# Optimization experiments

Measured on AMD Instinct MI355X. Metric: run time of the kernel, lower is better.

## Reference

```python
import jax, jax.numpy as jnp
import numpy as np

B, K, L, D, H = 128, 51, 60, 1, 32
NB = 2  # MAF blocks
LOG2PI = float(np.log(2.0 * np.pi))


def setup_inputs():
    kit = iter(jax.random.split(jax.random.key(0), 64))
    def nrm(shape, s=0.05):
        return jax.random.normal(next(kit), shape, dtype=jnp.float32) * s
    def uni(shape, lo, hi):
        return jax.random.uniform(next(kit), shape, dtype=jnp.float32, minval=lo, maxval=hi)
    c = L * D          # attention feature dim = 60
    KL = K * L         # 3060
    KL32 = KL * 32     # 97920
    return dict(
        x=jax.random.normal(next(kit), (B, K, L, D), dtype=jnp.float32),
        attn_Wq=nrm((c, c), 0.1), attn_bq=nrm((c,), 0.1),
        attn_Wk=nrm((c, c), 0.1), attn_bk=nrm((c,), 0.1),
        lstm_Wih=nrm((4 * H, D), 0.2), lstm_Whh=nrm((4 * H, H), 0.1),
        lstm_bih=nrm((4 * H,), 0.1), lstm_bhh=nrm((4 * H,), 0.1),
        gnn_Wn=nrm((H, H), 0.1), gnn_bn=nrm((H,), 0.1),
        gnn_Wr=nrm((H, H), 0.1),
        gnn_W2=nrm((H, H), 0.1), gnn_b2=nrm((H,), 0.1),
        mlp_W1=nrm((KL, 500), 0.02), mlp_b1=nrm((500,), 0.05),
        bn1_g=uni((500,), 0.8, 1.2), bn1_b=nrm((500,), 0.05),
        bn1_m=nrm((500,), 0.05), bn1_v=uni((500,), 0.5, 1.5),
        mlp_W2=nrm((500, 500), 0.05), mlp_b2=nrm((500,), 0.05),
        bn2_g=uni((500,), 0.8, 1.2), bn2_b=nrm((500,), 0.05),
        bn2_m=nrm((500,), 0.05), bn2_v=uni((500,), 0.5, 1.5),
        mlp_W3=nrm((500, KL32), 0.05), mlp_b3=nrm((KL32,), 0.05),
        ann_W=nrm((KL32, 100), 0.005), ann_b=nrm((100,), 0.05),
        annbn_g=uni((100,), 0.8, 1.2), annbn_b=nrm((100,), 0.05),
        annbn_m=nrm((100,), 0.05), annbn_v=uni((100,), 0.5, 1.5),
        maf_in_W=nrm((NB, H, D), 0.1), maf_in_b=nrm((NB, H), 0.1),
        maf_cond_W=nrm((NB, H, H), 0.1),
        maf_out_W=nrm((NB, 2 * D, H), 0.1), maf_out_b=nrm((NB, 2 * D), 0.1),
        maf_bn_lg=nrm((NB, D), 0.05), maf_bn_beta=nrm((NB, D), 0.05),
    )


def _forward(x, attn_Wq, attn_bq, attn_Wk, attn_bk,
             lstm_Wih, lstm_Whh, lstm_bih, lstm_bhh,
             gnn_Wn, gnn_bn, gnn_Wr, gnn_W2, gnn_b2,
             mlp_W1, mlp_b1, bn1_g, bn1_b, bn1_m, bn1_v,
             mlp_W2, mlp_b2, bn2_g, bn2_b, bn2_m, bn2_v,
             mlp_W3, mlp_b3,
             ann_W, ann_b, annbn_g, annbn_b, annbn_m, annbn_v,
             maf_in_W, maf_in_b, maf_cond_W, maf_out_W, maf_out_b,
             maf_bn_lg, maf_bn_beta):
    Bb, Kk, Ll, Dd = x.shape
    c = Ll * Dd
    # --- ScaleDotProductAttention (eval: dropout = identity) ---
    xf = x.reshape(Bb, Kk, c)
    q = xf @ attn_Wq + attn_bq
    k = xf @ attn_Wk + attn_bk
    k_t = k.reshape(Bb, c, Kk)                 # torch .view -- a reshape, NOT a transpose
    score = (q @ k_t) / jnp.sqrt(jnp.asarray(c, x.dtype))
    graph = jax.nn.softmax(score, axis=1)      # softmax over dim=1, (B,K,K)
    # --- single-layer LSTM over (B*K, L, D) ---
    xs = x.reshape(Bb * Kk, Ll, Dd)
    Hh = lstm_Whh.shape[1]
    def step(carry, xt):
        h, cc = carry
        z = xt @ lstm_Wih.T + lstm_bih + h @ lstm_Whh.T + lstm_bhh
        i, f, g, o = jnp.split(z, 4, axis=-1)  # torch gate order i,f,g,o
        cc = jax.nn.sigmoid(f) * cc + jax.nn.sigmoid(i) * jnp.tanh(g)
        h = jax.nn.sigmoid(o) * jnp.tanh(cc)
        return (h, cc), h
    h0 = jnp.zeros((Bb * Kk, Hh), dtype=x.dtype)
    _, hs = jax.lax.scan(step, (h0, h0), jnp.swapaxes(xs, 0, 1))
    h = jnp.swapaxes(hs, 0, 1).reshape(Bb, Kk, Ll, Hh)  # (B,K,L,H)
    # --- GNN message passing on attention-derived adjacency ---
    agg = jnp.einsum('bkld,bkj->bjld', h, graph)
    h_n = agg @ gnn_Wn + gnn_bn
    h_n = h_n.at[:, :, 1:].add(h[:, :, :-1] @ gnn_Wr)   # temporal shift residual
    h_gcn = jax.nn.relu(h_n) @ gnn_W2 + gnn_b2
    # --- gcn_mlp residual (BatchNorm1d in eval mode) ---
    bn = lambda z, g, b, m, v: (z - m) / jnp.sqrt(v + 1e-5) * g + b
    xflat = xs.reshape(Bb, -1)                          # (B, K*L*D)
    z = bn(jax.nn.relu(xflat @ mlp_W1 + mlp_b1), bn1_g, bn1_b, bn1_m, bn1_v)
    z = bn(jax.nn.relu(z @ mlp_W2 + mlp_b2), bn2_g, bn2_b, bn2_m, bn2_v)
    z = z @ mlp_W3 + mlp_b3
    h_gcn = z.reshape(h_gcn.shape) + h_gcn
    # --- ann head ---
    hid = bn(jax.nn.relu(h_gcn.reshape(Bb, -1) @ ann_W + ann_b),
             annbn_g, annbn_b, annbn_m, annbn_v)
    # --- conditional MAF log-prob over rows of (B*K*L, 1) with cond (., H) ---
    # input_size==1 => MADE output mask is all-zero (output degree -1 < hidden degree 0)
    u = xs.reshape(-1, Dd)
    cond = h_gcn.reshape(-1, h_gcn.shape[-1])
    mask_out = jnp.zeros((2 * Dd, Hh), dtype=x.dtype)
    sum_ldj = jnp.zeros_like(u)
    eps = 1e-5
    for i in range(maf_in_W.shape[0]):
        hm = jnp.tanh(u @ maf_in_W[i].T + maf_in_b[i] + cond @ maf_cond_W[i].T)
        out = hm @ (maf_out_W[i] * mask_out).T + maf_out_b[i]
        m, loga = out[:, :Dd], out[:, Dd:]
        u = (u - m) * jnp.exp(-loga)
        sum_ldj = sum_ldj - loga
        # flow BatchNorm, eval mode (running_mean=0, running_var=1 buffers)
        u = jnp.exp(maf_bn_lg[i]) * u * jax.lax.rsqrt(jnp.asarray(1.0 + eps, x.dtype)) + maf_bn_beta[i]
        sum_ldj = sum_ldj + maf_bn_lg[i] - 0.5 * jnp.log(jnp.asarray(1.0 + eps, x.dtype))
    logp_row = jnp.sum(-0.5 * LOG2PI - 0.5 * u * u + sum_ldj, axis=1)  # (B*K*L,)
    log_prob = logp_row.reshape(Bb, -1).mean(axis=1)    # (B,)
    return hid, log_prob, h_gcn


def reference(x, attn_Wq, attn_bq, attn_Wk, attn_bk,
              lstm_Wih, lstm_Whh, lstm_bih, lstm_bhh,
              gnn_Wn, gnn_bn, gnn_Wr, gnn_W2, gnn_b2,
              mlp_W1, mlp_b1, bn1_g, bn1_b, bn1_m, bn1_v,
              mlp_W2, mlp_b2, bn2_g, bn2_b, bn2_m, bn2_v,
              mlp_W3, mlp_b3,
              ann_W, ann_b, annbn_g, annbn_b, annbn_m, annbn_v,
              maf_in_W, maf_in_b, maf_cond_W, maf_out_W, maf_out_b,
              maf_bn_lg, maf_bn_beta):
    hid, log_prob, h_gcn = _forward(
        x, attn_Wq, attn_bq, attn_Wk, attn_bk,
        lstm_Wih, lstm_Whh, lstm_bih, lstm_bhh,
        gnn_Wn, gnn_bn, gnn_Wr, gnn_W2, gnn_b2,
        mlp_W1, mlp_b1, bn1_g, bn1_b, bn1_m, bn1_v,
        mlp_W2, mlp_b2, bn2_g, bn2_b, bn2_m, bn2_v,
        mlp_W3, mlp_b3,
        ann_W, ann_b, annbn_g, annbn_b, annbn_m, annbn_v,
        maf_in_W, maf_in_b, maf_cond_W, maf_out_W, maf_out_b,
        maf_bn_lg, maf_bn_beta)
    return (hid, log_prob.mean(), h_gcn, log_prob)
```

## Files before the change

### kernel.cpp

```cpp
#include <hip/hip_runtime.h>
#include <math.h>

constexpr int cB = 128;
constexpr int cK = 51;
constexpr int cL = 60;
constexpr int cH = 32;
constexpr int cC = 60;
constexpr int cKL = 3060;
constexpr int cKL32 = 97920;
constexpr float kLOG2PI = 1.8378770664093453f;

typedef __attribute__((ext_vector_type(8))) short bfrag8;
typedef __attribute__((ext_vector_type(16))) float accf16;
typedef __attribute__((ext_vector_type(4))) unsigned uint4v;

__device__ __forceinline__ float fsig(float x) { return 1.0f / (1.0f + __expf(-x)); }
__device__ __forceinline__ float ftanh(float x) {
  float e = __expf(2.0f * x);
  return 1.0f - 2.0f / (e + 1.0f);
}
__device__ __forceinline__ short f2bf(float f) {
  union { float f; unsigned u; } v; v.f = f;
  unsigned r = v.u + 0x7FFFu + ((v.u >> 16) & 1u);
  return (short)(r >> 16);
}
__device__ __forceinline__ unsigned pk2bf(float lo, float hi) {
  unsigned r;
  asm("v_cvt_pk_bf16_f32 %0, %1, %2" : "=v"(r) : "v"(lo), "v"(hi));
  return r;
}

__global__ __launch_bounds__(256) void qk_kernel(
    const float* __restrict__ x, const float* __restrict__ Wq, const float* __restrict__ bq,
    const float* __restrict__ Wk, const float* __restrict__ bk,
    float* __restrict__ q, float* __restrict__ kx) {
  __shared__ float xs[8][cC];
  const int row0 = blockIdx.x * 8;
  const int tid = threadIdx.x;
  for (int idx = tid; idx < 8 * cC; idx += 256) {
    int lr = idx / cC, t = idx % cC;
    xs[lr][t] = x[(row0 + lr) * cC + t];
  }
  __syncthreads();
  for (int idx = tid; idx < 8 * 2 * cC; idx += 256) {
    int col = idx % cC;
    int r2 = idx / cC;
    int m = r2 & 1, lr = r2 >> 1;
    const float* W = m ? Wk : Wq;
    float acc = m ? bk[col] : bq[col];
    #pragma unroll 4
    for (int t = 0; t < cC; ++t) acc += xs[lr][t] * W[t * cC + col];
    float* outp = m ? kx : q;
    outp[(row0 + lr) * cC + col] = acc;
  }
}

__global__ __launch_bounds__(256) void attn_kernel(
    const float* __restrict__ q, const float* __restrict__ kx, float* __restrict__ graph) {
  __shared__ float qb[cKL];
  __shared__ float kb[cKL];
  __shared__ float sc[cK * cK];
  __shared__ float cmax[cK], csum[cK];
  const int b = blockIdx.x;
  const int tid = threadIdx.x;
  for (int idx = tid; idx < cKL; idx += 256) {
    qb[idx] = q[b * cKL + idx];
    kb[idx] = kx[b * cKL + idx];
  }
  __syncthreads();
  const float scale = 1.0f / sqrtf(60.0f);
  for (int idx = tid; idx < cK * cK; idx += 256) {
    int i = idx / cK, j = idx % cK;
    float acc = 0.0f;
    #pragma unroll 4
    for (int t = 0; t < cC; ++t) acc += qb[i * cC + t] * kb[t * cK + j];
    sc[idx] = acc * scale;
  }
  __syncthreads();
  if (tid < cK) {
    float m = -1e30f;
    for (int i = 0; i < cK; ++i) m = fmaxf(m, sc[i * cK + tid]);
    float ssum = 0.0f;
    for (int i = 0; i < cK; ++i) ssum += __expf(sc[i * cK + tid] - m);
    cmax[tid] = m; csum[tid] = ssum;
  }
  __syncthreads();
  for (int idx = tid; idx < cK * cK; idx += 256) {
    int j = idx % cK;
    graph[b * cK * cK + idx] = __expf(sc[idx] - cmax[j]) / csum[j];
  }
}

__global__ __launch_bounds__(256) void lstm_kernel(
    const float* __restrict__ x, const float* __restrict__ Wih, const float* __restrict__ Whh,
    const float* __restrict__ bih, const float* __restrict__ bhh, float* __restrict__ hout) {
  const int wave = threadIdx.x >> 6;
  const int lane = threadIdx.x & 63;
  const int seq = blockIdx.x * 4 + wave;
  const int j = lane;
  float w0[32], w1[32];
  #pragma unroll
  for (int k2 = 0; k2 < 32; ++k2) {
    w0[k2] = Whh[j * 32 + k2];
    w1[k2] = Whh[(j + 64) * 32 + k2];
  }
  const float wi0 = Wih[j], wi1 = Wih[j + 64];
  const float bb0 = bih[j] + bhh[j];
  const float bb1 = bih[j + 64] + bhh[j + 64];
  const float xr = (lane < cL) ? x[seq * cL + lane] : 0.0f;
  float h = 0.0f, c = 0.0f;
  float* outp = hout + (size_t)seq * cL * cH;
  for (int t = 0; t < cL; ++t) {
    const float xt = __shfl(xr, t);
    float a0 = bb0 + wi0 * xt;
    float a1 = bb1 + wi1 * xt;
    #pragma unroll
    for (int k2 = 0; k2 < 32; ++k2) {
      const float hk = __shfl(h, k2);
      a0 += w0[k2] * hk;
      a1 += w1[k2] * hk;
    }
    const float sA = fsig(a0);
    const float sB = fsig(a1);
    const float tB = ftanh(a1);
    const float p = sA * tB;
    const float sf = __shfl(sA, (lane & 31) + 32);
    const float so = __shfl(sB, (lane & 31) + 32);
    c = sf * c + p;
    h = so * ftanh(c);
    if (lane < 32) outp[t * cH + lane] = h;
  }
}

__global__ __launch_bounds__(256) void agg_kernel(
    const float* __restrict__ hbuf, const float* __restrict__ graph,
    float* __restrict__ aggout) {
  __shared__ float G[cK * cK];
  __shared__ __align__(16) float Ht[cK][128];
  const int b = blockIdx.y;
  const int c0 = blockIdx.x * 128;
  const int tid = threadIdx.x;
  for (int idx = tid; idx < cK * cK; idx += 256) G[idx] = graph[b * cK * cK + idx];
  for (int idx = tid; idx < cK * 128; idx += 256) {
    int k = idx >> 7, c = idx & 127;
    Ht[k][c] = hbuf[((size_t)b * cK + k) * 1920 + c0 + c];
  }
  __syncthreads();
  const int jg = tid >> 5;
  const int cg = tid & 31;
  const int cc = cg * 4;
  float4 acc[7];
  #pragma unroll
  for (int jj = 0; jj < 7; ++jj) acc[jj] = make_float4(0.f, 0.f, 0.f, 0.f);
  for (int k = 0; k < cK; ++k) {
    const float4 hv = *reinterpret_cast<const float4*>(&Ht[k][cc]);
    #pragma unroll
    for (int jj = 0; jj < 7; ++jj) {
      const int j = jg + jj * 8;
      const float g = (j < cK) ? G[k * cK + j] : 0.0f;
      acc[jj].x += g * hv.x; acc[jj].y += g * hv.y;
      acc[jj].z += g * hv.z; acc[jj].w += g * hv.w;
    }
  }
  #pragma unroll
  for (int jj = 0; jj < 7; ++jj) {
    const int j = jg + jj * 8;
    if (j < cK) {
      const size_t o = ((size_t)b * cK + j) * 1920 + c0 + cc;
      aggout[o + 0] = acc[jj].x; aggout[o + 1] = acc[jj].y;
      aggout[o + 2] = acc[jj].z; aggout[o + 3] = acc[jj].w;
    }
  }
}

__global__ __launch_bounds__(256) void gnn2_kernel(
    const float* __restrict__ hbuf, const float* __restrict__ Wn,
    const float* __restrict__ bn_, const float* __restrict__ Wr,
    const float* __restrict__ W2, const float* __restrict__ b2,
    float* __restrict__ hg) {
  __shared__ __align__(16) float wn[cH * cH];
  __shared__ __align__(16) float wr[cH * cH];
  __shared__ __align__(16) float w2[cH * cH];
  __shared__ float bnb[cH], b2b[cH];
  __shared__ float A_[192][33];
  __shared__ float M_[192][33];
  const int tid = threadIdx.x;
  const int row0 = blockIdx.x * 192;
  for (int idx = tid; idx < cH * cH; idx += 256) { wn[idx] = Wn[idx]; wr[idx] = Wr[idx]; w2[idx] = W2[idx]; }
  if (tid < cH) { bnb[tid] = bn_[tid]; b2b[tid] = b2[tid]; }
  for (int idx = tid; idx < 192 * 32; idx += 256) {
    const int r = idx >> 5, d = idx & 31;
    A_[r][d] = hg[(size_t)(row0 + r) * 32 + d];
    const int g = row0 + r;
    const int l = g % 60;
    M_[r][d] = (l > 0) ? hbuf[(size_t)(g - 1) * 32 + d] : 0.0f;
  }
  __syncthreads();
  const int rg = tid >> 2;
  const int cg = tid & 3;
  const int c0 = cg * 8;
  const int r0 = rg * 3;
  float acc[3][8];
  #pragma unroll
  for (int i = 0; i < 3; ++i)
    #pragma unroll
    for (int d = 0; d < 8; ++d) acc[i][d] = bnb[c0 + d];
  for (int e = 0; e < cH; ++e) {
    const float4 wn0 = *reinterpret_cast<const float4*>(&wn[e * cH + c0]);
    const float4 wn1 = *reinterpret_cast<const float4*>(&wn[e * cH + c0 + 4]);
    const float4 wr0 = *reinterpret_cast<const float4*>(&wr[e * cH + c0]);
    const float4 wr1 = *reinterpret_cast<const float4*>(&wr[e * cH + c0 + 4]);
    #pragma unroll
    for (int i = 0; i < 3; ++i) {
      const float a = A_[r0 + i][e];
      const float m = M_[r0 + i][e];
      acc[i][0] += a * wn0.x + m * wr0.x; acc[i][1] += a * wn0.y + m * wr0.y;
      acc[i][2] += a * wn0.z + m * wr0.z; acc[i][3] += a * wn0.w + m * wr0.w;
      acc[i][4] += a * wn1.x + m * wr1.x; acc[i][5] += a * wn1.y + m * wr1.y;
      acc[i][6] += a * wn1.z + m * wr1.z; acc[i][7] += a * wn1.w + m * wr1.w;
    }
  }
  __syncthreads();
  #pragma unroll
  for (int i = 0; i < 3; ++i)
    #pragma unroll
    for (int d = 0; d < 8; ++d) A_[r0 + i][c0 + d] = fmaxf(acc[i][d], 0.0f);
  __syncthreads();
  float acc2[3][8];
  #pragma unroll
  for (int i = 0; i < 3; ++i)
    #pragma unroll
    for (int d = 0; d < 8; ++d) acc2[i][d] = b2b[c0 + d];
  for (int e = 0; e < cH; ++e) {
    const float4 w20 = *reinterpret_cast<const float4*>(&w2[e * cH + c0]);
    const float4 w21 = *reinterpret_cast<const float4*>(&w2[e * cH + c0 + 4]);
    #pragma unroll
    for (int i = 0; i < 3; ++i) {
      const float t = A_[r0 + i][e];
      acc2[i][0] += t * w20.x; acc2[i][1] += t * w20.y;
      acc2[i][2] += t * w20.z; acc2[i][3] += t * w20.w;
      acc2[i][4] += t * w21.x; acc2[i][5] += t * w21.y;
      acc2[i][6] += t * w21.z; acc2[i][7] += t * w21.w;
    }
  }
  #pragma unroll
  for (int i = 0; i < 3; ++i)
    #pragma unroll
    for (int d = 0; d < 8; ++d) M_[r0 + i][c0 + d] = acc2[i][d];
  __syncthreads();
  for (int idx = tid; idx < 192 * 32; idx += 256) {
    const int r = idx >> 5, d = idx & 31;
    hg[(size_t)row0 * 32 + idx] = M_[r][d];
  }
}

__global__ __launch_bounds__(256) void gemm_splitk_kernel(
    const float* __restrict__ A, const float* __restrict__ W,
    int K, int N, float* __restrict__ partial) {
  __shared__ __align__(16) float At[128][65];
  __shared__ __align__(16) float Wt[64][64];
  const int tid = threadIdx.x;
  const int n0 = blockIdx.x * 64;
  const int k0 = blockIdx.y * 64;
  const int kw = min(64, K - k0);
  for (int idx = tid; idx < 128 * 64; idx += 256) {
    int r = idx >> 6, kk = idx & 63;
    At[r][kk] = (kk < kw) ? A[(size_t)r * K + k0 + kk] : 0.0f;
  }
  for (int idx = tid; idx < 64 * 64; idx += 256) {
    int kk = idx >> 6, cc = idx & 63;
    Wt[kk][cc] = (kk < kw && n0 + cc < N) ? W[(size_t)(k0 + kk) * N + n0 + cc] : 0.0f;
  }
  __syncthreads();
  const int cg = tid & 15, rg = tid >> 4;
  const int c0 = cg * 4, r0 = rg * 8;
  float acc[8][4];
  #pragma unroll
  for (int i = 0; i < 8; ++i)
    #pragma unroll
    for (int jj = 0; jj < 4; ++jj) acc[i][jj] = 0.0f;
  for (int kk = 0; kk < 64; kk += 2) {
    const float4 wv0 = *reinterpret_cast<const float4*>(&Wt[kk][c0]);
    const float4 wv1 = *reinterpret_cast<const float4*>(&Wt[kk + 1][c0]);
    #pragma unroll
    for (int i = 0; i < 8; ++i) {
      const float2 av = *reinterpret_cast<const float2*>(&At[r0 + i][kk]);
      acc[i][0] += av.x * wv0.x + av.y * wv1.x;
      acc[i][1] += av.x * wv0.y + av.y * wv1.y;
      acc[i][2] += av.x * wv0.z + av.y * wv1.z;
      acc[i][3] += av.x * wv0.w + av.y * wv1.w;
    }
  }
  float* p = partial + (size_t)blockIdx.y * 128 * N;
  #pragma unroll
  for (int i = 0; i < 8; ++i) {
    #pragma unroll
    for (int jj = 0; jj < 4; ++jj) {
      const int cc = n0 + c0 + jj;
      if (cc < N) p[(r0 + i) * N + cc] = acc[i][jj];
    }
  }
}

__global__ __launch_bounds__(256) void mlpred_kernel(
    const float* __restrict__ partial, int S, int N,
    const float* __restrict__ bias, const float* __restrict__ gg,
    const float* __restrict__ bb, const float* __restrict__ mm,
    const float* __restrict__ vv, float* __restrict__ outz) {
  const int oi = blockIdx.x * 256 + threadIdx.x;
  if (oi >= 128 * N) return;
  float s = 0.0f;
  for (int p = 0; p < S; ++p) s += partial[(size_t)p * 128 * N + oi];
  const int c = oi % N;
  const float z = fmaxf(s + bias[c], 0.0f);
  outz[oi] = (z - mm[c]) * rsqrtf(vv[c] + 1e-5f) * gg[c] + bb[c];
}

__global__ __launch_bounds__(256) void mlpredbf_kernel(
    const float* __restrict__ partial, int S,
    const float* __restrict__ bias, const float* __restrict__ gg,
    const float* __restrict__ bb, const float* __restrict__ mm,
    const float* __restrict__ vv, unsigned short* __restrict__ outbf) {
  const int oi = blockIdx.x * 256 + threadIdx.x;
  if (oi >= 128 * 512) return;
  const int r = oi >> 9, c = oi & 511;
  unsigned short val = 0;
  if (c < 500) {
    float s = 0.0f;
    for (int p = 0; p < S; ++p) s += partial[(size_t)p * 64000 + r * 500 + c];
    const float z = fmaxf(s + bias[c], 0.0f);
    const float y = (z - mm[c]) * rsqrtf(vv[c] + 1e-5f) * gg[c] + bb[c];
    val = (unsigned short)f2bf(y);
  }
  outbf[oi] = val;
}

__global__ __launch_bounds__(256, 3) void w3_mfma_kernel(
    const unsigned short* __restrict__ z2bf, const float* __restrict__ W3,
    const float* __restrict__ b3, float* __restrict__ outh) {
  __shared__ unsigned Bs[2][16][128];
  const int tid = threadIdx.x;
  const int n0 = blockIdx.x * 128;
  const int wv = tid >> 6;
  const int lane = tid & 63;
  const int half = lane >> 5;
  const int lm = lane & 31;
  const int kp = tid >> 4;
  const int nc = (tid & 15) << 3;

  accf16 acc[4] = {};

  const unsigned short* Ab = z2bf + lm * 512 + half * 8;
  const float* Wp = W3 + (size_t)(2 * kp) * cKL32 + n0 + nc;

  {
    const float4 r0a = *reinterpret_cast<const float4*>(Wp);
    const float4 r0b = *reinterpret_cast<const float4*>(Wp + 4);
    const float4 r1a = *reinterpret_cast<const float4*>(Wp + cKL32);
    const float4 r1b = *reinterpret_cast<const float4*>(Wp + cKL32 + 4);
    uint4v w0 = {pk2bf(r0a.x, r1a.x), pk2bf(r0a.y, r1a.y), pk2bf(r0a.z, r1a.z), pk2bf(r0a.w, r1a.w)};
    uint4v w1 = {pk2bf(r0b.x, r1b.x), pk2bf(r0b.y, r1b.y), pk2bf(r0b.z, r1b.z), pk2bf(r0b.w, r1b.w)};
    *reinterpret_cast<uint4v*>(&Bs[0][kp][nc]) = w0;
    *reinterpret_cast<uint4v*>(&Bs[0][kp][nc + 4]) = w1;
  }
  __syncthreads();

  int cur = 0;
  for (int t = 0; t < 16; ++t) {
    const int k0 = t << 5;
    bfrag8 a0[4], a1[4];
    #pragma unroll
    for (int mf = 0; mf < 4; ++mf) {
      a0[mf] = *reinterpret_cast<const bfrag8*>(Ab + mf * 16384 + k0);
      a1[mf] = *reinterpret_cast<const bfrag8*>(Ab + mf * 16384 + k0 + 16);
    }
    float4 r0a = make_float4(0.f, 0.f, 0.f, 0.f), r0b = r0a, r1a = r0a, r1b = r0a;
    if (t < 15) {
      const int kA = k0 + 32 + 2 * kp;
      const float* p = Wp + (size_t)(k0 + 32) * cKL32;
      if (kA < 500)     { r0a = *reinterpret_cast<const float4*>(p);
                          r0b = *reinterpret_cast<const float4*>(p + 4); }
      if (kA + 1 < 500) { r1a = *reinterpret_cast<const float4*>(p + cKL32);
                          r1b = *reinterpret_cast<const float4*>(p + cKL32 + 4); }
    }
    const unsigned* Bf = &Bs[cur][0][0];
    const int colL = wv * 32 + lm;
    union { unsigned u[4]; bfrag8 b; } cv0, cv1;
    #pragma unroll
    for (int c = 0; c < 4; ++c) cv0.u[c] = Bf[(half * 4 + c) * 128 + colL];
    #pragma unroll
    for (int c = 0; c < 4; ++c) cv1.u[c] = Bf[(8 + half * 4 + c) * 128 + colL];
    #pragma unroll
    for (int mf = 0; mf < 4; ++mf)
      acc[mf] = __builtin_amdgcn_mfma_f32_32x32x16_bf16(a0[mf], cv0.b, acc[mf], 0, 0, 0);
    #pragma unroll
    for (int mf = 0; mf < 4; ++mf)
      acc[mf] = __builtin_amdgcn_mfma_f32_32x32x16_bf16(a1[mf], cv1.b, acc[mf], 0, 0, 0);
    if (t < 15) {
      uint4v w0 = {pk2bf(r0a.x, r1a.x), pk2bf(r0a.y, r1a.y), pk2bf(r0a.z, r1a.z), pk2bf(r0a.w, r1a.w)};
      uint4v w1 = {pk2bf(r0b.x, r1b.x), pk2bf(r0b.y, r1b.y), pk2bf(r0b.z, r1b.z), pk2bf(r0b.w, r1b.w)};
      *reinterpret_cast<uint4v*>(&Bs[cur ^ 1][kp][nc]) = w0;
      *reinterpret_cast<uint4v*>(&Bs[cur ^ 1][kp][nc + 4]) = w1;
    }
    __syncthreads();
    cur ^= 1;
  }

  const int col = n0 + wv * 32 + lm;
  const float bias = b3[col];
  #pragma unroll
  for (int mf = 0; mf < 4; ++mf) {
    #pragma unroll
    for (int reg = 0; reg < 16; ++reg) {
      const int rr = mf * 32 + (reg & 3) + 8 * (reg >> 2) + 4 * half;
      const size_t o = (size_t)rr * cKL32 + col;
      outh[o] += acc[mf][reg] + bias;
    }
  }
}

__global__ __launch_bounds__(256, 3) void ann_mfma_kernel(
    const float* __restrict__ hg, const float* __restrict__ annW,
    float* __restrict__ partial) {
  __shared__ unsigned Bs[2][16][128];
  const int tid = threadIdx.x;
  const int bx = blockIdx.x;
  const int kbase = bx * 128;
  const int wv = tid >> 6;
  const int lane = tid & 63;
  const int half = lane >> 5;
  const int lm = lane & 31;

  accf16 acc[4] = {};

  #pragma unroll
  for (int i = 0; i < 8; ++i) {
    const int idx = tid + i * 256;
    const int kp = idx >> 7, col = idx & 127;
    float w0 = 0.f, w1 = 0.f;
    if (col < 100) {
      const size_t base = (size_t)(kbase + 2 * kp) * 100 + col;
      w0 = annW[base];
      w1 = annW[base + 100];
    }
    Bs[0][kp][col] = pk2bf(w0, w1);
  }
  __syncthreads();

  const float* Ap = hg + (size_t)lm * cKL32 + kbase + half * 8;
  int cur = 0;
  for (int t = 0; t < 4; ++t) {
    const int k0 = t * 32;
    bfrag8 a0[4], a1[4];
    #pragma unroll
    for (int mf = 0; mf < 4; ++mf) {
      const float* p = Ap + (size_t)mf * 32 * cKL32 + k0;
      const float4 f0 = *reinterpret_cast<const float4*>(p);
      const float4 f1 = *reinterpret_cast<const float4*>(p + 4);
      const float4 g0 = *reinterpret_cast<const float4*>(p + 16);
      const float4 g1 = *reinterpret_cast<const float4*>(p + 20);
      union { unsigned u[4]; bfrag8 b; } ua, ub;
      ua.u[0] = pk2bf(f0.x, f0.y); ua.u[1] = pk2bf(f0.z, f0.w);
      ua.u[2] = pk2bf(f1.x, f1.y); ua.u[3] = pk2bf(f1.z, f1.w);
      ub.u[0] = pk2bf(g0.x, g0.y); ub.u[1] = pk2bf(g0.z, g0.w);
      ub.u[2] = pk2bf(g1.x, g1.y); ub.u[3] = pk2bf(g1.z, g1.w);
      a0[mf] = ua.b; a1[mf] = ub.b;
    }
    float w0r[8], w1r[8];
    if (t < 3) {
      #pragma unroll
      for (int i = 0; i < 8; ++i) {
        const int idx = tid + i * 256;
        const int kp = idx >> 7, col = idx & 127;
        w0r[i] = 0.f; w1r[i] = 0.f;
        if (col < 100) {
          const size_t base = (size_t)(kbase + (t + 1) * 32 + 2 * kp) * 100 + col;
          w0r[i] = annW[base];
          w1r[i] = annW[base + 100];
        }
      }
    }
    const unsigned* Bf = &Bs[cur][0][0];
    const int colL = wv * 32 + lm;
    union { unsigned u[4]; bfrag8 b; } cv0, cv1;
    #pragma unroll
    for (int c = 0; c < 4; ++c) cv0.u[c] = Bf[(half * 4 + c) * 128 + colL];
    #pragma unroll
    for (int c = 0; c < 4; ++c) cv1.u[c] = Bf[(8 + half * 4 + c) * 128 + colL];
    #pragma unroll
    for (int mf = 0; mf < 4; ++mf)
      acc[mf] = __builtin_amdgcn_mfma_f32_32x32x16_bf16(a0[mf], cv0.b, acc[mf], 0, 0, 0);
    #pragma unroll
    for (int mf = 0; mf < 4; ++mf)
      acc[mf] = __builtin_amdgcn_mfma_f32_32x32x16_bf16(a1[mf], cv1.b, acc[mf], 0, 0, 0);
    if (t < 3) {
      #pragma unroll
      for (int i = 0; i < 8; ++i) {
        const int idx = tid + i * 256;
        const int kp = idx >> 7, col = idx & 127;
        Bs[cur ^ 1][kp][col] = pk2bf(w0r[i], w1r[i]);
      }
    }
    __syncthreads();
    cur ^= 1;
  }

  const int col = wv * 32 + lm;
  if (col < 100) {
    float* p = partial + (size_t)bx * 12800;
    #pragma unroll
    for (int mf = 0; mf < 4; ++mf) {
      #pragma unroll
      for (int reg = 0; reg < 16; ++reg) {
        const int rr = mf * 32 + (reg & 3) + 8 * (reg >> 2) + 4 * half;
        p[rr * 100 + col] = acc[mf][reg];
      }
    }
  }
}

__global__ __launch_bounds__(256) void annred1_kernel(
    const float* __restrict__ partial, float* __restrict__ partial2) {
  const int oi = blockIdx.x * 256 + threadIdx.x;
  const int by = blockIdx.y;
  if (oi >= 12800) return;
  const float* p = partial + (size_t)(by * 51) * 12800 + oi;
  float s = 0.0f;
  #pragma unroll 4
  for (int q = 0; q < 51; ++q) s += p[(size_t)q * 12800];
  partial2[(size_t)by * 12800 + oi] = s;
}

__global__ __launch_bounds__(256) void annred2_kernel(
    const float* __restrict__ partial2, const float* __restrict__ ab,
    const float* __restrict__ gg, const float* __restrict__ bb,
    const float* __restrict__ mm, const float* __restrict__ vv, float* __restrict__ hid) {
  const int oi = blockIdx.x * 256 + threadIdx.x;
  if (oi < 12800) {
    float s = 0.0f;
    #pragma unroll
    for (int p = 0; p < 15; ++p) s += partial2[(size_t)p * 12800 + oi];
    const int c = oi % 100;
    const float z = fmaxf(s + ab[c], 0.0f);
    hid[oi] = (z - mm[c]) * rsqrtf(vv[c] + 1e-5f) * gg[c] + bb[c];
  }
}

__global__ __launch_bounds__(256) void logp_kernel(
    const float* __restrict__ x, const float* __restrict__ mob,
    const float* __restrict__ mlg, const float* __restrict__ mbeta, float* __restrict__ lp) {
  const int b = blockIdx.x;
  const int tid = threadIdx.x;
  const float rs = rsqrtf(1.0f + 1e-5f);
  const float A0 = __expf(mlg[0] - mob[1]) * rs;
  const float B0 = -mob[0] * __expf(-mob[1]) * __expf(mlg[0]) * rs + mbeta[0];
  const float A1 = __expf(mlg[1] - mob[3]) * rs;
  const float B1 = -mob[2] * __expf(-mob[3]) * __expf(mlg[1]) * rs + mbeta[1];
  const float S = (mlg[0] - mob[1]) + (mlg[1] - mob[3]) - logf(1.0f + 1e-5f);
  const float a = A1 * A0;
  const float bc = A1 * B0 + B1;
  float s = 0.0f;
  for (int t = tid; t < cKL; t += 256) {
    const float u = a * x[b * cKL + t] + bc;
    s += u * u;
  }
  #pragma unroll
  for (int off = 32; off > 0; off >>= 1) s += __shfl_down(s, off);
  __shared__ float red[4];
  if ((tid & 63) == 0) red[tid >> 6] = s;
  __syncthreads();
  if (tid == 0) {
    const float tot = red[0] + red[1] + red[2] + red[3];
    lp[b] = -0.5f * tot / (float)cKL + (-0.5f * kLOG2PI + S);
  }
}

__global__ void lpmean_kernel(const float* __restrict__ lp, float* __restrict__ outm) {
  __shared__ float red[128];
  const int tid = threadIdx.x;
  red[tid] = lp[tid];
  __syncthreads();
  for (int off = 64; off > 0; off >>= 1) {
    if (tid < off) red[tid] += red[tid + off];
    __syncthreads();
  }
  if (tid == 0) outm[0] = red[0] / 128.0f;
}

extern "C" void kernel_launch(void* const* d_in, const int* in_sizes, int n_in,
                              void* d_out, int out_size, void* d_ws, size_t ws_size,
                              hipStream_t stream) {
  const float* x    = (const float*)d_in[0];
  const float* Wq   = (const float*)d_in[1];
  const float* bq   = (const float*)d_in[2];
  const float* Wk   = (const float*)d_in[3];
  const float* bk   = (const float*)d_in[4];
  const float* Wih  = (const float*)d_in[5];
  const float* Whh  = (const float*)d_in[6];
  const float* bih  = (const float*)d_in[7];
  const float* bhh  = (const float*)d_in[8];
  const float* gWn  = (const float*)d_in[9];
  const float* gbn  = (const float*)d_in[10];
  const float* gWr  = (const float*)d_in[11];
  const float* gW2  = (const float*)d_in[12];
  const float* gb2  = (const float*)d_in[13];
  const float* W1   = (const float*)d_in[14];
  const float* b1   = (const float*)d_in[15];
  const float* bn1g = (const float*)d_in[16];
  const float* bn1b = (const float*)d_in[17];
  const float* bn1m = (const float*)d_in[18];
  const float* bn1v = (const float*)d_in[19];
  const float* W2m  = (const float*)d_in[20];
  const float* b2m  = (const float*)d_in[21];
  const float* bn2g = (const float*)d_in[22];
  const float* bn2b = (const float*)d_in[23];
  const float* bn2m = (const float*)d_in[24];
  const float* bn2v = (const float*)d_in[25];
  const float* W3   = (const float*)d_in[26];
  const float* b3   = (const float*)d_in[27];
  const float* annW = (const float*)d_in[28];
  const float* annb = (const float*)d_in[29];
  const float* abg  = (const float*)d_in[30];
  const float* abb  = (const float*)d_in[31];
  const float* abm  = (const float*)d_in[32];
  const float* abv  = (const float*)d_in[33];
  const float* mob  = (const float*)d_in[38];
  const float* mlg  = (const float*)d_in[39];
  const float* mbeta= (const float*)d_in[40];

  float* ws = (float*)d_ws;
  float* qb    = ws;
  float* kb    = ws + 391680;
  float* graph = ws + 783360;
  float* hbuf  = ws + 1116288;
  float* z1    = ws + 13650048;
  unsigned short* z2bf = (unsigned short*)(ws + 13714048);
  float* partial  = hbuf;
  float* partial2 = hbuf + 10000000;
  float* mp    = hbuf + 4000000;

  float* outF = (float*)d_out;
  float* hid  = outF;
  float* lpm  = outF + 12800;
  float* hgcn = outF + 12801;
  float* lp   = outF + 12546561;

  qk_kernel<<<816, 256, 0, stream>>>(x, Wq, bq, Wk, bk, qb, kb);
  attn_kernel<<<128, 256, 0, stream>>>(qb, kb, graph);
  lstm_kernel<<<1632, 256, 0, stream>>>(x, Wih, Whh, bih, bhh, hbuf);
  agg_kernel<<<dim3(15, 128), 256, 0, stream>>>(hbuf, graph, hgcn);
  gnn2_kernel<<<2040, 256, 0, stream>>>(hbuf, gWn, gbn, gWr, gW2, gb2, hgcn);
  gemm_splitk_kernel<<<dim3(8, 48), 256, 0, stream>>>(x, W1, 3060, 500, mp);
  mlpred_kernel<<<250, 256, 0, stream>>>(mp, 48, 500, b1, bn1g, bn1b, bn1m, bn1v, z1);
  gemm_splitk_kernel<<<dim3(8, 8), 256, 0, stream>>>(z1, W2m, 500, 500, mp);
  mlpredbf_kernel<<<256, 256, 0, stream>>>(mp, 8, b2m, bn2g, bn2b, bn2m, bn2v, z2bf);
  w3_mfma_kernel<<<765, 256, 0, stream>>>(z2bf, W3, b3, hgcn);
  ann_mfma_kernel<<<765, 256, 0, stream>>>(hgcn, annW, partial);
  annred1_kernel<<<dim3(50, 15), 256, 0, stream>>>(partial, partial2);
  annred2_kernel<<<50, 256, 0, stream>>>(partial2, annb, abg, abb, abm, abv, hid);
  logp_kernel<<<128, 256, 0, stream>>>(x, mob, mlg, mbeta, lp);
  lpmean_kernel<<<1, 128, 0, stream>>>(lp, lpm);
}
```

Measured before the change: 860.2 us.

## Run LSTM recurrence on bf16 MFMA with 16 sequences per wave

Rewrites the LSTM kernel so each single-wave block advances 16 sequences together. The hidden-to-gate product becomes eight 16x16x32 bf16 MFMAs per timestep, with the hidden state exchanged through LDS instead of 32 shuffles per step per sequence. Sigmoid and tanh now use the hardware reciprocal instead of a divide. The cost is bf16 rounding of weights and hidden state, which can drift over 60 steps, plus two barriers per step and a grid of only 408 single-wave blocks.

```diff
diff --git a/kernel.cpp b/kernel.cpp
--- a/kernel.cpp
+++ b/kernel.cpp
@@ -12,12 +12,14 @@
 
 typedef __attribute__((ext_vector_type(8))) short bfrag8;
 typedef __attribute__((ext_vector_type(16))) float accf16;
+typedef __attribute__((ext_vector_type(4))) float accf4;
 typedef __attribute__((ext_vector_type(4))) unsigned uint4v;
 
-__device__ __forceinline__ float fsig(float x) { return 1.0f / (1.0f + __expf(-x)); }
+__device__ __forceinline__ float frcp(float x) { return __builtin_amdgcn_rcpf(x); }
+__device__ __forceinline__ float fsig(float x) { return frcp(1.0f + __expf(-x)); }
 __device__ __forceinline__ float ftanh(float x) {
   float e = __expf(2.0f * x);
-  return 1.0f - 2.0f / (e + 1.0f);
+  return 1.0f - 2.0f * frcp(e + 1.0f);
 }
 __device__ __forceinline__ short f2bf(float f) {
   union { float f; unsigned u; } v; v.f = f;
@@ -91,44 +93,77 @@
   }
 }
 
-__global__ __launch_bounds__(256) void lstm_kernel(
+__global__ __launch_bounds__(64) void lstm_mfma_kernel(
     const float* __restrict__ x, const float* __restrict__ Wih, const float* __restrict__ Whh,
     const float* __restrict__ bih, const float* __restrict__ bhh, float* __restrict__ hout) {
-  const int wave = threadIdx.x >> 6;
-  const int lane = threadIdx.x & 63;
-  const int seq = blockIdx.x * 4 + wave;
-  const int j = lane;
-  float w0[32], w1[32];
-  #pragma unroll
-  for (int k2 = 0; k2 < 32; ++k2) {
-    w0[k2] = Whh[j * 32 + k2];
-    w1[k2] = Whh[(j + 64) * 32 + k2];
-  }
-  const float wi0 = Wih[j], wi1 = Wih[j + 64];
-  const float bb0 = bih[j] + bhh[j];
-  const float bb1 = bih[j + 64] + bhh[j + 64];
-  const float xr = (lane < cL) ? x[seq * cL + lane] : 0.0f;
-  float h = 0.0f, c = 0.0f;
-  float* outp = hout + (size_t)seq * cL * cH;
+  __shared__ float xlds[cL][16];
+  __shared__ __align__(16) float hlds[16][36];
+  const int lane = threadIdx.x;
+  const int n = lane & 15;
+  const int grp = lane >> 4;
+  const int seq0 = blockIdx.x * 16;
+
+  for (int i = lane; i < 16 * cL; i += 64) {
+    const int s = i / cL, t = i % cL;
+    xlds[t][s] = x[(size_t)(seq0 + s) * cL + t];
+  }
+  for (int i = lane; i < 16 * 36; i += 64) (&hlds[0][0])[i] = 0.0f;
+
+  bfrag8 bf[8];
+  float bias8[8], wih8[8];
+  #pragma unroll
+  for (int g = 0; g < 8; ++g) {
+    const float* wrow = Whh + (g * 16 + n) * cH + grp * 8;
+    const float4 p0 = *reinterpret_cast<const float4*>(wrow);
+    const float4 p1 = *reinterpret_cast<const float4*>(wrow + 4);
+    union { unsigned u[4]; bfrag8 b; } ub;
+    ub.u[0] = pk2bf(p0.x, p0.y); ub.u[1] = pk2bf(p0.z, p0.w);
+    ub.u[2] = pk2bf(p1.x, p1.y); ub.u[3] = pk2bf(p1.z, p1.w);
+    bf[g] = ub.b;
+    bias8[g] = bih[g * 16 + n] + bhh[g * 16 + n];
+    wih8[g] = Wih[g * 16 + n];
+  }
+  float cst[8];
+  #pragma unroll
+  for (int i = 0; i < 8; ++i) cst[i] = 0.0f;
+  __syncthreads();
+
+  float* outp = hout + (size_t)seq0 * cL * cH;
   for (int t = 0; t < cL; ++t) {
-    const float xt = __shfl(xr, t);
-    float a0 = bb0 + wi0 * xt;
-    float a1 = bb1 + wi1 * xt;
-    #pragma unroll
-    for (int k2 = 0; k2 < 32; ++k2) {
-      const float hk = __shfl(h, k2);
-      a0 += w0[k2] * hk;
-      a1 += w1[k2] * hk;
-    }
-    const float sA = fsig(a0);
-    const float sB = fsig(a1);
-    const float tB = ftanh(a1);
-    const float p = sA * tB;
-    const float sf = __shfl(sA, (lane & 31) + 32);
-    const float so = __shfl(sB, (lane & 31) + 32);
-    c = sf * c + p;
-    h = so * ftanh(c);
-    if (lane < 32) outp[t * cH + lane] = h;
+    const float4 h0 = *reinterpret_cast<const float4*>(&hlds[n][grp * 8]);
+    const float4 h1 = *reinterpret_cast<const float4*>(&hlds[n][grp * 8 + 4]);
+    union { unsigned u[4]; bfrag8 b; } ua;
+    ua.u[0] = pk2bf(h0.x, h0.y); ua.u[1] = pk2bf(h0.z, h0.w);
+    ua.u[2] = pk2bf(h1.x, h1.y); ua.u[3] = pk2bf(h1.z, h1.w);
+    const float4 xt = *reinterpret_cast<const float4*>(&xlds[t][grp * 4]);
+    accf4 acc[8];
+    #pragma unroll
+    for (int g = 0; g < 8; ++g) {
+      accf4 ci;
+      ci[0] = fmaf(wih8[g], xt.x, bias8[g]);
+      ci[1] = fmaf(wih8[g], xt.y, bias8[g]);
+      ci[2] = fmaf(wih8[g], xt.z, bias8[g]);
+      ci[3] = fmaf(wih8[g], xt.w, bias8[g]);
+      acc[g] = __builtin_amdgcn_mfma_f32_16x16x32_bf16(ua.b, bf[g], ci, 0, 0, 0);
+    }
+    __syncthreads();
+    #pragma unroll
+    for (int hh = 0; hh < 2; ++hh) {
+      #pragma unroll
+      for (int r = 0; r < 4; ++r) {
+        const float iv = acc[0 + hh][r];
+        const float fv = acc[2 + hh][r];
+        const float gv = acc[4 + hh][r];
+        const float ov = acc[6 + hh][r];
+        float cs = cst[hh * 4 + r];
+        cs = fmaf(fsig(fv), cs, fsig(iv) * ftanh(gv));
+        const float hv = fsig(ov) * ftanh(cs);
+        cst[hh * 4 + r] = cs;
+        hlds[grp * 4 + r][n + hh * 16] = hv;
+        outp[(size_t)(grp * 4 + r) * (cL * cH) + t * cH + n + hh * 16] = hv;
+      }
+    }
+    __syncthreads();
   }
 }
 
@@ -647,7 +682,7 @@
 
   qk_kernel<<<816, 256, 0, stream>>>(x, Wq, bq, Wk, bk, qb, kb);
   attn_kernel<<<128, 256, 0, stream>>>(qb, kb, graph);
-  lstm_kernel<<<1632, 256, 0, stream>>>(x, Wih, Whh, bih, bhh, hbuf);
+  lstm_mfma_kernel<<<408, 64, 0, stream>>>(x, Wih, Whh, bih, bhh, hbuf);
   agg_kernel<<<dim3(15, 128), 256, 0, stream>>>(hbuf, graph, hgcn);
   gnn2_kernel<<<2040, 256, 0, stream>>>(hbuf, gWn, gbn, gWr, gW2, gb2, hgcn);
   gemm_splitk_kernel<<<dim3(8, 48), 256, 0, stream>>>(x, W1, 3060, 500, mp);
```

Result: faster. 750.8 us (-12.7%).
